# Optimization experiments

Measured on AMD Instinct MI355X. Metric: run time of the kernel, lower is better.

## Reference

```python
import jax, jax.numpy as jnp
import numpy as np

EMBED = 512
HEADS = 8
HEAD_DIM = EMBED // HEADS


def setup_inputs() -> dict:
    key = jax.random.key(0)
    ks = jax.random.split(key, 9)
    N, L = 4, 2048
    values = jax.random.normal(ks[0], (N, L, EMBED), dtype=jnp.float32)
    keys = jax.random.normal(ks[1], (N, L, EMBED), dtype=jnp.float32)
    query = jax.random.normal(ks[2], (N, L, EMBED), dtype=jnp.float32)
    mask = jax.random.randint(ks[3], (N, 1, 1, L), 0, 2, dtype=jnp.int32)
    s_h = 1.0 / np.sqrt(HEAD_DIM).astype(np.float32)
    s_e = 1.0 / np.sqrt(EMBED).astype(np.float32)
    Wv = jax.random.normal(ks[4], (HEAD_DIM, HEAD_DIM), dtype=jnp.float32) * s_h
    Wk = jax.random.normal(ks[5], (HEAD_DIM, HEAD_DIM), dtype=jnp.float32) * s_h
    Wq = jax.random.normal(ks[6], (HEAD_DIM, HEAD_DIM), dtype=jnp.float32) * s_h
    Wo = jax.random.normal(ks[7], (EMBED, EMBED), dtype=jnp.float32) * s_e
    bo = jnp.zeros((EMBED,), dtype=jnp.float32)
    return {"values": values, "keys": keys, "query": query, "mask": mask,
            "Wv": Wv, "Wk": Wk, "Wq": Wq, "Wo": Wo, "bo": bo}


def reference(values, keys, query, mask, Wv, Wk, Wq, Wo, bo):
    N, Lq, E = query.shape
    D = Wv.shape[0]
    H = E // D
    Lk = keys.shape[1]
    # split heads: [N, L, H, D]
    v = values.reshape(N, values.shape[1], H, D)
    k = keys.reshape(N, Lk, H, D)
    q = query.reshape(N, Lq, H, D)
    # per-head linear projections (nn.Linear: x @ W^T, no bias)
    v = jnp.einsum("nlhd,ed->nlhe", v, Wv)
    k = jnp.einsum("nlhd,ed->nlhe", k, Wk)
    q = jnp.einsum("nlhd,ed->nlhe", q, Wq)
    # energy: [N, H, Lq, Lk]
    energy = jnp.einsum("nqhd,nkhd->nhqk", q, k)
    energy = jnp.where(mask == 0, jnp.float32(-1e20), energy)
    # NOTE: original scales by sqrt(embed_size), not sqrt(head_dim)
    attn = jax.nn.softmax(energy / jnp.sqrt(jnp.float32(E)), axis=3)
    out = jnp.einsum("nhqk,nkhd->nqhd", attn, v).reshape(N, Lq, E)
    return out @ Wo.T + bo
```

## Files before the change

### kernel.cpp

```cpp
#include <hip/hip_runtime.h>

#define LSEQ 2048
#define EMB  512
#define NH   8
#define HD   64
#define NBATCH 4
#define QSCALE (0.044194173824159216f * 1.4426950408889634f)

using short8  = __attribute__((ext_vector_type(8))) short;
using short4v = __attribute__((ext_vector_type(4))) short;
using f32x4   = __attribute__((ext_vector_type(4))) float;

__device__ __forceinline__ short bf16r(float f) {
  union { float f; unsigned u; } x; x.f = f;
  unsigned r = x.u + 0x7FFFu + ((x.u >> 16) & 1u);
  return (short)(r >> 16);
}

__device__ __forceinline__ float exp2v(float x) {
  float r;
  asm("v_exp_f32 %0, %1" : "=v"(r) : "v"(x));
  return r;
}

__device__ __forceinline__ unsigned cvtpk(float lo, float hi) {
  unsigned r;
  asm("v_cvt_pk_bf16_f32 %0, %1, %2" : "=v"(r) : "v"(lo), "v"(hi));
  return r;
}

__device__ __forceinline__ void stage16(const void* g, void* l) {
  __builtin_amdgcn_global_load_lds(
      (const __attribute__((address_space(1))) unsigned int*)g,
      (__attribute__((address_space(3))) unsigned int*)l, 16, 0, 0);
}

__device__ __forceinline__ short8 cvt8(const float* __restrict__ p) {
  float4 a = ((const float4*)p)[0];
  float4 b = ((const float4*)p)[1];
  short8 r;
  r[0]=bf16r(a.x); r[1]=bf16r(a.y); r[2]=bf16r(a.z); r[3]=bf16r(a.w);
  r[4]=bf16r(b.x); r[5]=bf16r(b.y); r[6]=bf16r(b.z); r[7]=bf16r(b.w);
  return r;
}

__device__ __forceinline__ short8 ld8(const short* __restrict__ p) {
  return *(const short8*)p;
}

__global__ __launch_bounds__(256) void prep_kernel(
    const int* __restrict__ mask, float* __restrict__ fbias,
    int* __restrict__ kidx, int* __restrict__ meta,
    const float* __restrict__ Wq, const float* __restrict__ Wk,
    const float* __restrict__ Wv, short* __restrict__ Wqb,
    short* __restrict__ Wkb, short* __restrict__ Wvb) {
  __shared__ int ssum[256];
  int b = blockIdx.x;
  int tid = threadIdx.x;
  if (b < 4) {
    int n = b;
    int base = n * LSEQ;
    int loc[8], c = 0;
#pragma unroll
    for (int j = 0; j < 8; j++) { loc[j] = mask[base + tid * 8 + j] != 0; c += loc[j]; }
    ssum[tid] = c;
    __syncthreads();
    for (int off = 1; off < 256; off <<= 1) {
      int v = (tid >= off) ? ssum[tid - off] : 0;
      __syncthreads();
      ssum[tid] += v;
      __syncthreads();
    }
    int total = ssum[255];
    int excl = ssum[tid] - c;
    int qz = (total == 0);
#pragma unroll
    for (int j = 0; j < 8; j++) {
      int i = tid * 8 + j;
      kidx[base + i] = qz ? i : 0;
      fbias[base + i] = (qz || i < total) ? 0.f : -1e30f;
    }
    __syncthreads();
    if (!qz) {
      int pos = excl;
#pragma unroll
      for (int j = 0; j < 8; j++)
        if (loc[j]) { kidx[base + pos] = tid * 8 + j; pos++; }
    }
    if (tid == 0) {
      meta[n] = qz ? (LSEQ / 64) : ((total + 63) >> 6);
      meta[4 + n] = qz;
    }
  } else {
    int t = (b - 4) >> 2;
    int i = ((b - 4) & 3) * 256 + tid;
    const float* W = (t == 0) ? Wq : (t == 1) ? Wk : Wv;
    short* O = (t == 0) ? Wqb : (t == 1) ? Wkb : Wvb;
    float sc = (t == 0) ? QSCALE : 1.f;
    float4 v = ((const float4*)W)[i];
    short4v r;
    r[0]=bf16r(v.x*sc); r[1]=bf16r(v.y*sc); r[2]=bf16r(v.z*sc); r[3]=bf16r(v.w*sc);
    ((short4v*)O)[i] = r;
  }
}

__global__ __launch_bounds__(256) void proj_kernel(
    const float* __restrict__ query, const float* __restrict__ keys,
    const float* __restrict__ values,
    const short* __restrict__ Wqb, const short* __restrict__ Wkb,
    const short* __restrict__ Wvb, const int* __restrict__ kidx,
    const int* __restrict__ meta,
    short* __restrict__ Qp, short* __restrict__ Kp, short* __restrict__ Vt) {
  __shared__ short tile[64][72];
  int t = blockIdx.y;
  const float* x = (t == 0) ? query : (t == 1) ? keys : values;
  const short* W = (t == 0) ? Wqb   : (t == 1) ? Wkb  : Wvb;
  int idx = blockIdx.x;
  int lt = idx & 31, h = (idx >> 5) & 7, n = idx >> 8;
  int tid = threadIdx.x, lane = tid & 63, w = tid >> 6;
  int row16 = lane & 15, g = lane >> 4;
  int lbase = lt * 64 + w * 16;

  int zq = 0;
  const float* xr;
  int lrow = lbase + row16;
  if (t == 0) {
    zq = meta[4 + n];
    xr = x + ((size_t)(n * LSEQ + lrow)) * EMB + h * HD + g * 8;
  } else {
    if (lbase >= ((meta[n] + 1) & ~1) * 64) return;
    int gidx = kidx[n * LSEQ + lrow];
    xr = x + ((size_t)(n * LSEQ + gidx)) * EMB + h * HD + g * 8;
  }
  short8 a0 = cvt8(xr);
  short8 a1 = cvt8(xr + 32);

  f32x4 acc[4];
#pragma unroll
  for (int et = 0; et < 4; et++) acc[et] = (f32x4){0.f, 0.f, 0.f, 0.f};
#pragma unroll
  for (int et = 0; et < 4; et++) {
    const short* wr = W + (size_t)(et * 16 + row16) * HD + g * 8;
    short8 b0 = ld8(wr);
    short8 b1 = ld8(wr + 32);
    acc[et] = __builtin_amdgcn_mfma_f32_16x16x32_bf16(a0, b0, acc[et], 0, 0, 0);
    acc[et] = __builtin_amdgcn_mfma_f32_16x16x32_bf16(a1, b1, acc[et], 0, 0, 0);
  }
  if (zq) {
#pragma unroll
    for (int et = 0; et < 4; et++) acc[et] = (f32x4){0.f, 0.f, 0.f, 0.f};
  }

  if (t == 2) {
#pragma unroll
    for (int et = 0; et < 4; et++)
#pragma unroll
      for (int r = 0; r < 4; r++)
        tile[et * 16 + row16][w * 16 + g * 4 + r] = bf16r(acc[et][r]);
  } else {
#pragma unroll
    for (int et = 0; et < 4; et++)
#pragma unroll
      for (int r = 0; r < 4; r++)
        tile[w * 16 + g * 4 + r][et * 16 + row16] = bf16r(acc[et][r]);
  }
  __syncthreads();

  size_t nh = (size_t)(n * NH + h);
#pragma unroll
  for (int i = tid; i < 512; i += 256) {
    int rr = i >> 3, cc = i & 7;
    short8 v = *(const short8*)&tile[rr][cc * 8];
    if (t == 2)
      *(short8*)(Vt + (nh * HD + rr) * LSEQ + lt * 64 + cc * 8) = v;
    else {
      short* O = (t == 0) ? Qp : Kp;
      *(short8*)(O + (nh * LSEQ + lt * 64 + rr) * HD + cc * 8) = v;
    }
  }
}

__global__ __launch_bounds__(256, 2) void attn_kernel(
    const short* __restrict__ Qp, const short* __restrict__ Kp,
    const short* __restrict__ Vt, const float* __restrict__ fbias,
    const int* __restrict__ meta, short* __restrict__ aout,
    const float* __restrict__ Wo, short* __restrict__ Wob) {
  __shared__ __align__(16) char smem[81920];

  int idx = blockIdx.x;
  int tid = threadIdx.x;
  if (idx >= NBATCH * NH * (LSEQ / 128)) {
    int i = (idx - NBATCH * NH * (LSEQ / 128)) * 256 + tid;
    float4 v = ((const float4*)Wo)[i];
    short4v r;
    r[0]=bf16r(v.x); r[1]=bf16r(v.y); r[2]=bf16r(v.z); r[3]=bf16r(v.w);
    ((short4v*)Wob)[i] = r;
    return;
  }
  int h = idx & 7;
  int qt = (idx >> 3) & 15;
  int n = idx >> 7;
  int lane = tid & 63, w = tid >> 6;
  int q0 = lane & 15, g = lane >> 4;
  int xr = q0 & 7;
  int nkt = (meta[n] + 1) >> 1;

  size_t nh = (size_t)(n * NH + h);
  const short* Qb = Qp + (nh * LSEQ + qt * 128 + w * 32) * HD;
  short8 bq00 = ld8(Qb + q0 * HD + g * 8);
  short8 bq01 = ld8(Qb + q0 * HD + 32 + g * 8);
  short8 bq10 = ld8(Qb + (16 + q0) * HD + g * 8);
  short8 bq11 = ld8(Qb + (16 + q0) * HD + 32 + g * 8);

  f32x4 acc0[4], acc1[4];
#pragma unroll
  for (int dt = 0; dt < 4; dt++) {
    acc0[dt] = (f32x4){0.f, 0.f, 0.f, 0.f};
    acc1[dt] = (f32x4){0.f, 0.f, 0.f, 0.f};
  }
  float l0 = 0.f, l1 = 0.f;

  const char* Ksrc = (const char*)(Kp + nh * (size_t)LSEQ * HD);
  const char* Vsrc = (const char*)(Vt + nh * (size_t)HD * LSEQ);
  const float* fb  = fbias + n * LSEQ + g * 4;

  int ksoff[4], vsoff[4], ldo[4];
#pragma unroll
  for (int j = 0; j < 4; j++) {
    int c = j * 256 + w * 64 + lane;
    int rK = c >> 3, cwK = (c & 7) ^ (rK & 7);
    ksoff[j] = rK * 128 + cwK * 16;
    int rV = c >> 4, cwV = c & 15;
    int sub = (cwV & 7) ^ (rV & 7);
    vsoff[j] = rV * (LSEQ * 2) + ((cwV & 8) + sub) * 16;
    ldo[j] = (j * 256 + w * 64) * 16;
  }

  int kfragb = q0 * 128 + ((g ^ xr) << 4);
  int vfragb = q0 * 256 + ((g ^ xr) << 4);
  int pbase = 65536 + w * 4096 + q0 * 128;
  char* pw_[4];
#pragma unroll
  for (int ks = 0; ks < 4; ks++)
    pw_[ks] = smem + pbase + ((ks * 32 + g * 8) ^ (xr << 4));
  const char* pr0 = smem + pbase + ((g * 16) ^ (xr << 4));
  const char* pr1 = smem + pbase + ((64 + g * 16) ^ (xr << 4));

#pragma unroll
  for (int j = 0; j < 4; j++) stage16(Ksrc + ksoff[j], smem + ldo[j]);
#pragma unroll
  for (int j = 0; j < 4; j++) stage16(Vsrc + vsoff[j], smem + 32768 + ldo[j]);
  __syncthreads();

  for (int kt = 0; kt < nkt; kt++) {
    int buf = kt & 1;
    if (kt < nkt - 1) {
      int bo = (buf ^ 1) * 16384;
      const char* Kn = Ksrc + (size_t)(kt + 1) * (128 * 128);
      const char* Vn = Vsrc + (size_t)(kt + 1) * 256;
#pragma unroll
      for (int j = 0; j < 4; j++) stage16(Kn + ksoff[j], smem + bo + ldo[j]);
#pragma unroll
      for (int j = 0; j < 4; j++) stage16(Vn + vsoff[j], smem + 32768 + bo + ldo[j]);
    }

#pragma unroll
    for (int h2 = 0; h2 < 2; h2++) {
      f32x4 fbv[4];
#pragma unroll
      for (int ks = 0; ks < 4; ks++)
        fbv[ks] = *(const f32x4*)(fb + kt * 128 + h2 * 64 + ks * 16);

      int kb_l = buf * 16384 + h2 * 8192 + kfragb;
      f32x4 s0[4], s1[4];
      __builtin_amdgcn_s_setprio(1);
#pragma unroll
      for (int ks = 0; ks < 4; ks++) {
        short8 k0 = *(const short8*)(smem + (kb_l + ks * 2048));
        short8 k1 = *(const short8*)(smem + ((kb_l + ks * 2048) ^ 64));
        f32x4 t0 = __builtin_amdgcn_mfma_f32_16x16x32_bf16(k0, bq00, fbv[ks], 0, 0, 0);
        s0[ks]   = __builtin_amdgcn_mfma_f32_16x16x32_bf16(k1, bq01, t0, 0, 0, 0);
        f32x4 t1 = __builtin_amdgcn_mfma_f32_16x16x32_bf16(k0, bq10, fbv[ks], 0, 0, 0);
        s1[ks]   = __builtin_amdgcn_mfma_f32_16x16x32_bf16(k1, bq11, t1, 0, 0, 0);
      }
      __builtin_amdgcn_s_setprio(0);

      float ps0 = 0.f, ps1 = 0.f;
#pragma unroll
      for (int ks = 0; ks < 4; ks++) {
        float p0 = exp2v(s0[ks][0] - 32.f), p1 = exp2v(s0[ks][1] - 32.f);
        float p2 = exp2v(s0[ks][2] - 32.f), p3 = exp2v(s0[ks][3] - 32.f);
        ps0 += (p0 + p1) + (p2 + p3);
        *(int2*)pw_[ks] = make_int2((int)cvtpk(p0, p1), (int)cvtpk(p2, p3));
        float q1 = exp2v(s1[ks][0] - 32.f), q2 = exp2v(s1[ks][1] - 32.f);
        float q3 = exp2v(s1[ks][2] - 32.f), q4 = exp2v(s1[ks][3] - 32.f);
        ps1 += (q1 + q2) + (q3 + q4);
        *(int2*)(pw_[ks] + 2048) = make_int2((int)cvtpk(q1, q2), (int)cvtpk(q3, q4));
      }
      l0 += ps0; l1 += ps1;

      asm volatile("s_waitcnt lgkmcnt(0)" ::: "memory");

      short8 ap00 = *(const short8*)pr0;
      short8 ap01 = *(const short8*)pr1;
      short8 ap10 = *(const short8*)(pr0 + 2048);
      short8 ap11 = *(const short8*)(pr1 + 2048);
      int vb_l = 32768 + buf * 16384 + vfragb + h2 * 128;
      __builtin_amdgcn_s_setprio(1);
#pragma unroll
      for (int dt = 0; dt < 4; dt++) {
        short8 v0 = *(const short8*)(smem + (vb_l + dt * 4096));
        short8 v1 = *(const short8*)(smem + ((vb_l + dt * 4096) ^ 64));
        acc0[dt] = __builtin_amdgcn_mfma_f32_16x16x32_bf16(ap00, v0, acc0[dt], 0, 0, 0);
        acc0[dt] = __builtin_amdgcn_mfma_f32_16x16x32_bf16(ap01, v1, acc0[dt], 0, 0, 0);
        acc1[dt] = __builtin_amdgcn_mfma_f32_16x16x32_bf16(ap10, v0, acc1[dt], 0, 0, 0);
        acc1[dt] = __builtin_amdgcn_mfma_f32_16x16x32_bf16(ap11, v1, acc1[dt], 0, 0, 0);
      }
      __builtin_amdgcn_s_setprio(0);
    }

    __syncthreads();
  }

  l0 += __shfl_xor(l0, 16);  l0 += __shfl_xor(l0, 32);
  l1 += __shfl_xor(l1, 16);  l1 += __shfl_xor(l1, 32);
  float li0 = l0 > 0.f ? 1.f / l0 : 0.f;
  float li1 = l1 > 0.f ? 1.f / l1 : 0.f;
  int lb = lane & 48;
  float w0[4], w1[4];
#pragma unroll
  for (int r = 0; r < 4; r++) {
    w0[r] = __shfl(li0, lb + g * 4 + r);
    w1[r] = __shfl(li1, lb + g * 4 + r);
  }
  int qrow = qt * 128 + w * 32;
#pragma unroll
  for (int r = 0; r < 4; r++) {
    size_t o0 = ((size_t)(n * LSEQ + qrow + g * 4 + r)) * EMB + h * HD;
    size_t o1 = ((size_t)(n * LSEQ + qrow + 16 + g * 4 + r)) * EMB + h * HD;
#pragma unroll
    for (int dt = 0; dt < 4; dt++) {
      aout[o0 + dt * 16 + q0] = bf16r(acc0[dt][r] * w0[r]);
      aout[o1 + dt * 16 + q0] = bf16r(acc1[dt][r] * w1[r]);
    }
  }
}

__global__ __launch_bounds__(256) void outproj_kernel(
    const short* __restrict__ aout, const short* __restrict__ Wob,
    const float* __restrict__ bo, float* __restrict__ out) {
  int mt = blockIdx.x, nt = blockIdx.y;
  int tid = threadIdx.x, lane = tid & 63, w = tid >> 6;
  int row16 = lane & 15, g = lane >> 4;
  int mrow = mt * 256 + w * 64;

  f32x4 acc[4][4];
#pragma unroll
  for (int hh = 0; hh < 4; hh++)
#pragma unroll
    for (int et = 0; et < 4; et++) acc[hh][et] = (f32x4){0.f, 0.f, 0.f, 0.f};

  for (int kc = 0; kc < 16; kc++) {
    short8 a[4];
#pragma unroll
    for (int hh = 0; hh < 4; hh++)
      a[hh] = ld8(aout + (size_t)(mrow + hh * 16 + row16) * EMB + kc * 32 + g * 8);
#pragma unroll
    for (int et = 0; et < 4; et++) {
      short8 b = ld8(Wob + (size_t)(nt * 64 + et * 16 + row16) * EMB + kc * 32 + g * 8);
#pragma unroll
      for (int hh = 0; hh < 4; hh++)
        acc[hh][et] = __builtin_amdgcn_mfma_f32_16x16x32_bf16(a[hh], b, acc[hh][et], 0, 0, 0);
    }
  }
#pragma unroll
  for (int et = 0; et < 4; et++) {
    int e = nt * 64 + et * 16 + row16;
    float bias = bo[e];
#pragma unroll
    for (int hh = 0; hh < 4; hh++)
#pragma unroll
      for (int r = 0; r < 4; r++)
        out[(size_t)(mrow + hh * 16 + g * 4 + r) * EMB + e] = acc[hh][et][r] + bias;
  }
}

extern "C" void kernel_launch(void* const* d_in, const int* in_sizes, int n_in,
                              void* d_out, int out_size, void* d_ws, size_t ws_size,
                              hipStream_t stream) {
  const float* values = (const float*)d_in[0];
  const float* keys   = (const float*)d_in[1];
  const float* query  = (const float*)d_in[2];
  const int*   mask   = (const int*)d_in[3];
  const float* Wv     = (const float*)d_in[4];
  const float* Wk     = (const float*)d_in[5];
  const float* Wq     = (const float*)d_in[6];
  const float* Wo     = (const float*)d_in[7];
  const float* bo     = (const float*)d_in[8];
  float* out = (float*)d_out;

  short* Qp = (short*)d_out;
  short* Kp = (short*)((char*)d_out + (8u << 20));
  char* ws = (char*)d_ws;
  short* Vt    = (short*)(ws);
  short* aout  = (short*)(ws + (8u << 20));
  short* Wob   = (short*)(ws + (16u << 20));
  float* fbias = (float*)(ws + (16u << 20) + (512u << 10));
  int*   kidx  = (int*)  (ws + (16u << 20) + (544u << 10));
  int*   meta  = (int*)  (ws + (16u << 20) + (576u << 10));
  short* Wqb   = (short*)(ws + (16u << 20) + (577u << 10));
  short* Wkb   = (short*)(ws + (16u << 20) + (585u << 10));
  short* Wvb   = (short*)(ws + (16u << 20) + (593u << 10));

  prep_kernel<<<16, 256, 0, stream>>>(mask, fbias, kidx, meta,
                                      Wq, Wk, Wv, Wqb, Wkb, Wvb);
  proj_kernel<<<dim3(NBATCH * NH * (LSEQ / 64), 3), 256, 0, stream>>>(
      query, keys, values, Wqb, Wkb, Wvb, kidx, meta, Qp, Kp, Vt);
  attn_kernel<<<NBATCH * NH * (LSEQ / 128) + 256, 256, 0, stream>>>(
      Qp, Kp, Vt, fbias, meta, aout, Wo, Wob);
  outproj_kernel<<<dim3((NBATCH * LSEQ) / 256, EMB / 64), 256, 0, stream>>>(
      aout, Wob, bo, out);
}
```

Measured before the change: 83.56 us.

## Fuse all four stages into one cooperative persistent kernel with grid syncs

Replaces the four separate launches (prep, projection, attention, output projection) with a single cooperative kernel of 512 blocks that runs each stage in turn, separated by grid-wide barriers. Launch gaps and per-kernel ramp-up and tail costs are removed. The output projection tiles are also reshaped to 128x64 per block, using two accumulator sets. In exchange, each stage is limited to 512 co-resident blocks with 80KB shared memory each, the grid syncs add their own cost, and the old multi-kernel path is kept as a fallback if the cooperative launch fails.

```diff
diff --git a/kernel.cpp b/kernel.cpp
--- a/kernel.cpp
+++ b/kernel.cpp
@@ -1,4 +1,7 @@
 #include <hip/hip_runtime.h>
+#include <hip/hip_cooperative_groups.h>
+
+namespace cg = cooperative_groups;
 
 #define LSEQ 2048
 #define EMB  512
@@ -47,6 +50,7 @@
 __device__ __forceinline__ short8 ld8(const short* __restrict__ p) {
   return *(const short8*)p;
 }
+
 
 __global__ __launch_bounds__(256) void prep_kernel(
     const int* __restrict__ mask, float* __restrict__ fbias,
@@ -367,10 +371,10 @@
       a[hh] = ld8(aout + (size_t)(mrow + hh * 16 + row16) * EMB + kc * 32 + g * 8);
 #pragma unroll
     for (int et = 0; et < 4; et++) {
-      short8 b = ld8(Wob + (size_t)(nt * 64 + et * 16 + row16) * EMB + kc * 32 + g * 8);
+      short8 bw = ld8(Wob + (size_t)(nt * 64 + et * 16 + row16) * EMB + kc * 32 + g * 8);
 #pragma unroll
       for (int hh = 0; hh < 4; hh++)
-        acc[hh][et] = __builtin_amdgcn_mfma_f32_16x16x32_bf16(a[hh], b, acc[hh][et], 0, 0, 0);
+        acc[hh][et] = __builtin_amdgcn_mfma_f32_16x16x32_bf16(a[hh], bw, acc[hh][et], 0, 0, 0);
     }
   }
 #pragma unroll
@@ -382,6 +386,329 @@
 #pragma unroll
       for (int r = 0; r < 4; r++)
         out[(size_t)(mrow + hh * 16 + g * 4 + r) * EMB + e] = acc[hh][et][r] + bias;
+  }
+}
+
+__global__ __launch_bounds__(256, 2) void fused_kernel(
+    const float* __restrict__ query, const float* __restrict__ keys,
+    const float* __restrict__ values, const int* __restrict__ mask,
+    const float* __restrict__ Wq, const float* __restrict__ Wk,
+    const float* __restrict__ Wv, const float* __restrict__ Wo,
+    const float* __restrict__ bo, short* __restrict__ Qp,
+    short* __restrict__ Kp, short* __restrict__ Vt, short* __restrict__ aout,
+    short* __restrict__ Wqb, short* __restrict__ Wkb, short* __restrict__ Wvb,
+    short* __restrict__ Wob, float* __restrict__ fbias, int* __restrict__ kidx,
+    int* __restrict__ meta, float* __restrict__ out) {
+  __shared__ __align__(16) char smem[81920];
+  int b = blockIdx.x, tid = threadIdx.x;
+
+  if (b < 4) {
+    int* ssum = (int*)smem;
+    int n = b, base = n * LSEQ;
+    int loc[8], c = 0;
+#pragma unroll
+    for (int j = 0; j < 8; j++) { loc[j] = mask[base + tid * 8 + j] != 0; c += loc[j]; }
+    ssum[tid] = c;
+    __syncthreads();
+    for (int off = 1; off < 256; off <<= 1) {
+      int v = (tid >= off) ? ssum[tid - off] : 0;
+      __syncthreads();
+      ssum[tid] += v;
+      __syncthreads();
+    }
+    int total = ssum[255], excl = ssum[tid] - c, qz = (total == 0);
+#pragma unroll
+    for (int j = 0; j < 8; j++) {
+      int i = tid * 8 + j;
+      kidx[base + i] = qz ? i : 0;
+      fbias[base + i] = (qz || i < total) ? 0.f : -1e30f;
+    }
+    __syncthreads();
+    if (!qz) {
+      int pos = excl;
+#pragma unroll
+      for (int j = 0; j < 8; j++)
+        if (loc[j]) { kidx[base + pos] = tid * 8 + j; pos++; }
+    }
+    if (tid == 0) {
+      meta[n] = qz ? (LSEQ / 64) : ((total + 63) >> 6);
+      meta[4 + n] = qz;
+    }
+  } else if (b < 16) {
+    int t = (b - 4) >> 2;
+    int i = ((b - 4) & 3) * 256 + tid;
+    const float* W = (t == 0) ? Wq : (t == 1) ? Wk : Wv;
+    short* O = (t == 0) ? Wqb : (t == 1) ? Wkb : Wvb;
+    float sc = (t == 0) ? QSCALE : 1.f;
+    float4 v = ((const float4*)W)[i];
+    short4v r;
+    r[0]=bf16r(v.x*sc); r[1]=bf16r(v.y*sc); r[2]=bf16r(v.z*sc); r[3]=bf16r(v.w*sc);
+    ((short4v*)O)[i] = r;
+  } else if (b < 272) {
+    int i = (b - 16) * 256 + tid;
+    float4 v = ((const float4*)Wo)[i];
+    short4v r;
+    r[0]=bf16r(v.x); r[1]=bf16r(v.y); r[2]=bf16r(v.z); r[3]=bf16r(v.w);
+    ((short4v*)Wob)[i] = r;
+  }
+  cg::this_grid().sync();
+
+  {
+    short (*tile)[72] = (short(*)[72])smem;
+    int lane = tid & 63, w = tid >> 6;
+    int row16 = lane & 15, g = lane >> 4;
+    for (int it = 0; it < 6; it++) {
+      int u = b + (it << 9);
+      int t = u >> 10, pidx = u & 1023;
+      int lt = pidx & 31, h = (pidx >> 5) & 7, n = pidx >> 8;
+      if (t != 0 && lt * 64 >= ((meta[n] + 1) & ~1) * 64) continue;
+      const float* x = (t == 0) ? query : (t == 1) ? keys : values;
+      const short* W = (t == 0) ? Wqb   : (t == 1) ? Wkb  : Wvb;
+      int lbase = lt * 64 + w * 16;
+      int lrow = lbase + row16;
+      int zq = 0;
+      const float* xr;
+      if (t == 0) {
+        zq = meta[4 + n];
+        xr = x + ((size_t)(n * LSEQ + lrow)) * EMB + h * HD + g * 8;
+      } else {
+        int gidx = kidx[n * LSEQ + lrow];
+        xr = x + ((size_t)(n * LSEQ + gidx)) * EMB + h * HD + g * 8;
+      }
+      short8 a0 = cvt8(xr);
+      short8 a1 = cvt8(xr + 32);
+
+      f32x4 acc[4];
+#pragma unroll
+      for (int et = 0; et < 4; et++) acc[et] = (f32x4){0.f, 0.f, 0.f, 0.f};
+#pragma unroll
+      for (int et = 0; et < 4; et++) {
+        const short* wr = W + (size_t)(et * 16 + row16) * HD + g * 8;
+        short8 b0 = ld8(wr);
+        short8 b1 = ld8(wr + 32);
+        acc[et] = __builtin_amdgcn_mfma_f32_16x16x32_bf16(a0, b0, acc[et], 0, 0, 0);
+        acc[et] = __builtin_amdgcn_mfma_f32_16x16x32_bf16(a1, b1, acc[et], 0, 0, 0);
+      }
+      if (zq) {
+#pragma unroll
+        for (int et = 0; et < 4; et++) acc[et] = (f32x4){0.f, 0.f, 0.f, 0.f};
+      }
+
+      if (t == 2) {
+#pragma unroll
+        for (int et = 0; et < 4; et++)
+#pragma unroll
+          for (int r = 0; r < 4; r++)
+            tile[et * 16 + row16][w * 16 + g * 4 + r] = bf16r(acc[et][r]);
+      } else {
+#pragma unroll
+        for (int et = 0; et < 4; et++)
+#pragma unroll
+          for (int r = 0; r < 4; r++)
+            tile[w * 16 + g * 4 + r][et * 16 + row16] = bf16r(acc[et][r]);
+      }
+      __syncthreads();
+
+      size_t nh = (size_t)(n * NH + h);
+      for (int i = tid; i < 512; i += 256) {
+        int rr = i >> 3, cc = i & 7;
+        short8 v = *(const short8*)&tile[rr][cc * 8];
+        if (t == 2)
+          *(short8*)(Vt + (nh * HD + rr) * LSEQ + lt * 64 + cc * 8) = v;
+        else {
+          short* O = (t == 0) ? Qp : Kp;
+          *(short8*)(O + (nh * LSEQ + lt * 64 + rr) * HD + cc * 8) = v;
+        }
+      }
+      __syncthreads();
+    }
+  }
+  cg::this_grid().sync();
+
+  {
+    int h = b & 7;
+    int qt = (b >> 3) & 15;
+    int n = b >> 7;
+    int lane = tid & 63, w = tid >> 6;
+    int q0 = lane & 15, g = lane >> 4;
+    int xr = q0 & 7;
+    int nkt = (meta[n] + 1) >> 1;
+
+    size_t nh = (size_t)(n * NH + h);
+    const short* Qb = Qp + (nh * LSEQ + qt * 128 + w * 32) * HD;
+    short8 bq00 = ld8(Qb + q0 * HD + g * 8);
+    short8 bq01 = ld8(Qb + q0 * HD + 32 + g * 8);
+    short8 bq10 = ld8(Qb + (16 + q0) * HD + g * 8);
+    short8 bq11 = ld8(Qb + (16 + q0) * HD + 32 + g * 8);
+
+    f32x4 acc0[4], acc1[4];
+#pragma unroll
+    for (int dt = 0; dt < 4; dt++) {
+      acc0[dt] = (f32x4){0.f, 0.f, 0.f, 0.f};
+      acc1[dt] = (f32x4){0.f, 0.f, 0.f, 0.f};
+    }
+    float l0 = 0.f, l1 = 0.f;
+
+    const char* Ksrc = (const char*)(Kp + nh * (size_t)LSEQ * HD);
+    const char* Vsrc = (const char*)(Vt + nh * (size_t)HD * LSEQ);
+    const float* fb  = fbias + n * LSEQ + g * 4;
+
+    int ksoff[4], vsoff[4], ldo[4];
+#pragma unroll
+    for (int j = 0; j < 4; j++) {
+      int c = j * 256 + w * 64 + lane;
+      int rK = c >> 3, cwK = (c & 7) ^ (rK & 7);
+      ksoff[j] = rK * 128 + cwK * 16;
+      int rV = c >> 4, cwV = c & 15;
+      int sub = (cwV & 7) ^ (rV & 7);
+      vsoff[j] = rV * (LSEQ * 2) + ((cwV & 8) + sub) * 16;
+      ldo[j] = (j * 256 + w * 64) * 16;
+    }
+
+    int kfragb = q0 * 128 + ((g ^ xr) << 4);
+    int vfragb = q0 * 256 + ((g ^ xr) << 4);
+    int pbase = 65536 + w * 4096 + q0 * 128;
+    char* pw_[4];
+#pragma unroll
+    for (int ks = 0; ks < 4; ks++)
+      pw_[ks] = smem + pbase + ((ks * 32 + g * 8) ^ (xr << 4));
+    const char* pr0 = smem + pbase + ((g * 16) ^ (xr << 4));
+    const char* pr1 = smem + pbase + ((64 + g * 16) ^ (xr << 4));
+
+#pragma unroll
+    for (int j = 0; j < 4; j++) stage16(Ksrc + ksoff[j], smem + ldo[j]);
+#pragma unroll
+    for (int j = 0; j < 4; j++) stage16(Vsrc + vsoff[j], smem + 32768 + ldo[j]);
+    __syncthreads();
+
+    for (int kt = 0; kt < nkt; kt++) {
+      int buf = kt & 1;
+      if (kt < nkt - 1) {
+        int bo2 = (buf ^ 1) * 16384;
+        const char* Kn = Ksrc + (size_t)(kt + 1) * (128 * 128);
+        const char* Vn = Vsrc + (size_t)(kt + 1) * 256;
+#pragma unroll
+        for (int j = 0; j < 4; j++) stage16(Kn + ksoff[j], smem + bo2 + ldo[j]);
+#pragma unroll
+        for (int j = 0; j < 4; j++) stage16(Vn + vsoff[j], smem + 32768 + bo2 + ldo[j]);
+      }
+
+#pragma unroll
+      for (int h2 = 0; h2 < 2; h2++) {
+        f32x4 fbv[4];
+#pragma unroll
+        for (int ks = 0; ks < 4; ks++)
+          fbv[ks] = *(const f32x4*)(fb + kt * 128 + h2 * 64 + ks * 16);
+
+        int kb_l = buf * 16384 + h2 * 8192 + kfragb;
+        f32x4 s0[4], s1[4];
+        __builtin_amdgcn_s_setprio(1);
+#pragma unroll
+        for (int ks = 0; ks < 4; ks++) {
+          short8 k0 = *(const short8*)(smem + (kb_l + ks * 2048));
+          short8 k1 = *(const short8*)(smem + ((kb_l + ks * 2048) ^ 64));
+          f32x4 t0 = __builtin_amdgcn_mfma_f32_16x16x32_bf16(k0, bq00, fbv[ks], 0, 0, 0);
+          s0[ks]   = __builtin_amdgcn_mfma_f32_16x16x32_bf16(k1, bq01, t0, 0, 0, 0);
+          f32x4 t1 = __builtin_amdgcn_mfma_f32_16x16x32_bf16(k0, bq10, fbv[ks], 0, 0, 0);
+          s1[ks]   = __builtin_amdgcn_mfma_f32_16x16x32_bf16(k1, bq11, t1, 0, 0, 0);
+        }
+        __builtin_amdgcn_s_setprio(0);
+
+        float ps0 = 0.f, ps1 = 0.f;
+#pragma unroll
+        for (int ks = 0; ks < 4; ks++) {
+          float p0 = exp2v(s0[ks][0] - 32.f), p1 = exp2v(s0[ks][1] - 32.f);
+          float p2 = exp2v(s0[ks][2] - 32.f), p3 = exp2v(s0[ks][3] - 32.f);
+          ps0 += (p0 + p1) + (p2 + p3);
+          *(int2*)pw_[ks] = make_int2((int)cvtpk(p0, p1), (int)cvtpk(p2, p3));
+          float q1 = exp2v(s1[ks][0] - 32.f), q2 = exp2v(s1[ks][1] - 32.f);
+          float q3 = exp2v(s1[ks][2] - 32.f), q4 = exp2v(s1[ks][3] - 32.f);
+          ps1 += (q1 + q2) + (q3 + q4);
+          *(int2*)(pw_[ks] + 2048) = make_int2((int)cvtpk(q1, q2), (int)cvtpk(q3, q4));
+        }
+        l0 += ps0; l1 += ps1;
+
+        asm volatile("s_waitcnt lgkmcnt(0)" ::: "memory");
+
+        short8 ap00 = *(const short8*)pr0;
+        short8 ap01 = *(const short8*)pr1;
+        short8 ap10 = *(const short8*)(pr0 + 2048);
+        short8 ap11 = *(const short8*)(pr1 + 2048);
+        int vb_l = 32768 + buf * 16384 + vfragb + h2 * 128;
+        __builtin_amdgcn_s_setprio(1);
+#pragma unroll
+        for (int dt = 0; dt < 4; dt++) {
+          short8 v0 = *(const short8*)(smem + (vb_l + dt * 4096));
+          short8 v1 = *(const short8*)(smem + ((vb_l + dt * 4096) ^ 64));
+          acc0[dt] = __builtin_amdgcn_mfma_f32_16x16x32_bf16(ap00, v0, acc0[dt], 0, 0, 0);
+          acc0[dt] = __builtin_amdgcn_mfma_f32_16x16x32_bf16(ap01, v1, acc0[dt], 0, 0, 0);
+          acc1[dt] = __builtin_amdgcn_mfma_f32_16x16x32_bf16(ap10, v0, acc1[dt], 0, 0, 0);
+          acc1[dt] = __builtin_amdgcn_mfma_f32_16x16x32_bf16(ap11, v1, acc1[dt], 0, 0, 0);
+        }
+        __builtin_amdgcn_s_setprio(0);
+      }
+
+      __syncthreads();
+    }
+
+    l0 += __shfl_xor(l0, 16);  l0 += __shfl_xor(l0, 32);
+    l1 += __shfl_xor(l1, 16);  l1 += __shfl_xor(l1, 32);
+    float li0 = l0 > 0.f ? 1.f / l0 : 0.f;
+    float li1 = l1 > 0.f ? 1.f / l1 : 0.f;
+    int lb = lane & 48;
+    float w0[4], w1[4];
+#pragma unroll
+    for (int r = 0; r < 4; r++) {
+      w0[r] = __shfl(li0, lb + g * 4 + r);
+      w1[r] = __shfl(li1, lb + g * 4 + r);
+    }
+    int qrow = qt * 128 + w * 32;
+#pragma unroll
+    for (int r = 0; r < 4; r++) {
+      size_t o0 = ((size_t)(n * LSEQ + qrow + g * 4 + r)) * EMB + h * HD;
+      size_t o1 = ((size_t)(n * LSEQ + qrow + 16 + g * 4 + r)) * EMB + h * HD;
+#pragma unroll
+      for (int dt = 0; dt < 4; dt++) {
+        aout[o0 + dt * 16 + q0] = bf16r(acc0[dt][r] * w0[r]);
+        aout[o1 + dt * 16 + q0] = bf16r(acc1[dt][r] * w1[r]);
+      }
+    }
+  }
+  cg::this_grid().sync();
+
+  {
+    int lane = tid & 63, w = tid >> 6;
+    int row16 = lane & 15, g = lane >> 4;
+    int mt = b >> 3, nt = b & 7;
+    int mrow = mt * 128 + w * 32;
+
+    f32x4 acc0[4], acc1[4];
+#pragma unroll
+    for (int et = 0; et < 4; et++) {
+      acc0[et] = (f32x4){0.f, 0.f, 0.f, 0.f};
+      acc1[et] = (f32x4){0.f, 0.f, 0.f, 0.f};
+    }
+
+    for (int kc = 0; kc < 16; kc++) {
+      short8 a0 = ld8(aout + (size_t)(mrow + row16) * EMB + kc * 32 + g * 8);
+      short8 a1 = ld8(aout + (size_t)(mrow + 16 + row16) * EMB + kc * 32 + g * 8);
+#pragma unroll
+      for (int et = 0; et < 4; et++) {
+        short8 bw = ld8(Wob + (size_t)(nt * 64 + et * 16 + row16) * EMB + kc * 32 + g * 8);
+        acc0[et] = __builtin_amdgcn_mfma_f32_16x16x32_bf16(a0, bw, acc0[et], 0, 0, 0);
+        acc1[et] = __builtin_amdgcn_mfma_f32_16x16x32_bf16(a1, bw, acc1[et], 0, 0, 0);
+      }
+    }
+#pragma unroll
+    for (int et = 0; et < 4; et++) {
+      int e = nt * 64 + et * 16 + row16;
+      float bias = bo[e];
+#pragma unroll
+      for (int r = 0; r < 4; r++) {
+        out[(size_t)(mrow + g * 4 + r) * EMB + e] = acc0[et][r] + bias;
+        out[(size_t)(mrow + 16 + g * 4 + r) * EMB + e] = acc1[et][r] + bias;
+      }
+    }
   }
 }
 
@@ -412,12 +739,23 @@
   short* Wkb   = (short*)(ws + (16u << 20) + (585u << 10));
   short* Wvb   = (short*)(ws + (16u << 20) + (593u << 10));
 
-  prep_kernel<<<16, 256, 0, stream>>>(mask, fbias, kidx, meta,
-                                      Wq, Wk, Wv, Wqb, Wkb, Wvb);
-  proj_kernel<<<dim3(NBATCH * NH * (LSEQ / 64), 3), 256, 0, stream>>>(
-      query, keys, values, Wqb, Wkb, Wvb, kidx, meta, Qp, Kp, Vt);
-  attn_kernel<<<NBATCH * NH * (LSEQ / 128) + 256, 256, 0, stream>>>(
-      Qp, Kp, Vt, fbias, meta, aout, Wo, Wob);
-  outproj_kernel<<<dim3((NBATCH * LSEQ) / 256, EMB / 64), 256, 0, stream>>>(
-      aout, Wob, bo, out);
-}
+  void* kargs[] = {
+      (void*)&query, (void*)&keys, (void*)&values, (void*)&mask,
+      (void*)&Wq, (void*)&Wk, (void*)&Wv, (void*)&Wo, (void*)&bo,
+      (void*)&Qp, (void*)&Kp, (void*)&Vt, (void*)&aout,
+      (void*)&Wqb, (void*)&Wkb, (void*)&Wvb, (void*)&Wob,
+      (void*)&fbias, (void*)&kidx, (void*)&meta, (void*)&out};
+  hipError_t cerr = hipLaunchCooperativeKernel(
+      (const void*)fused_kernel, dim3(512), dim3(256), kargs, 0, stream);
+  if (cerr != hipSuccess) {
+    (void)hipGetLastError();
+    prep_kernel<<<16, 256, 0, stream>>>(mask, fbias, kidx, meta,
+                                        Wq, Wk, Wv, Wqb, Wkb, Wvb);
+    proj_kernel<<<dim3(NBATCH * NH * (LSEQ / 64), 3), 256, 0, stream>>>(
+        query, keys, values, Wqb, Wkb, Wvb, kidx, meta, Qp, Kp, Vt);
+    attn_kernel<<<NBATCH * NH * (LSEQ / 128) + 256, 256, 0, stream>>>(
+        Qp, Kp, Vt, fbias, meta, aout, Wo, Wob);
+    outproj_kernel<<<dim3((NBATCH * LSEQ) / 256, EMB / 64), 256, 0, stream>>>(
+        aout, Wob, bo, out);
+  }
+}
```

Measured after the change: 268.3 us. 221% more time.
